# Optimization experiments

Measured on AMD Instinct MI355X. Metric: run time of the kernel, lower is better.

The kernel has to match this reference:

```python
import jax, jax.numpy as jnp
import numpy as np

HEADS = 12
DIM_HEAD = 64
SCALE = DIM_HEAD ** -0.5


def _attn(q, k, v):
    # q: [B, I, D], k/v: [B, J, D]
    sim = jnp.einsum('bid,bjd->bij', q, k)
    a = jax.nn.softmax(sim, axis=-1)
    out = jnp.einsum('bij,bjd->bid', a, v)
    return out, a


def setup_inputs() -> dict:
    key = jax.random.key(0)
    k1, k2, k3 = jax.random.split(key, 3)
    B, F, N, DIM = 8, 8, 196, 768
    x = jax.random.normal(k1, (B, 1 + F * N, DIM), dtype=jnp.float32)
    W_qkv = jax.random.normal(k2, (DIM, 3 * HEADS * DIM_HEAD), dtype=jnp.float32) * (DIM ** -0.5)
    W_out = jax.random.normal(k3, (HEADS * DIM_HEAD, DIM), dtype=jnp.float32) * ((HEADS * DIM_HEAD) ** -0.5)
    b_out = jnp.zeros((DIM,), dtype=jnp.float32)
    return {"x": x, "W_qkv": W_qkv, "W_out": W_out, "b_out": b_out, "f": F}


def reference(x, W_qkv, W_out, b_out, f):
    b, n_tot, dim = x.shape
    h, d = HEADS, DIM_HEAD
    qkv = x @ W_qkv                              # [b, n, 3*h*d]
    q, k, v = jnp.split(qkv, 3, axis=-1)
    # 'b n (h d) -> (b h) n d'
    def to_bh(t):
        return t.reshape(b, n_tot, h, d).transpose(0, 2, 1, 3).reshape(b * h, n_tot, d)
    q, k, v = map(to_bh, (q, k, v))
    q = q * SCALE
    cls_q, q_ = q[:, :1], q[:, 1:]
    cls_k, k_ = k[:, :1], k[:, 1:]
    cls_v, v_ = v[:, :1], v[:, 1:]
    # cls token attends over full sequence
    cls_out, cls_attn = _attn(cls_q, k, v)       # [(b h), 1, d], [(b h), 1, n_tot]
    # spatial attention: 'b (f n) d -> (b f) n d'
    bh = b * h
    n = (n_tot - 1) // f
    def to_bf(t):
        return t.reshape(bh, f, n, d).reshape(bh * f, n, d)
    q_, k_, v_ = map(to_bf, (q_, k_, v_))
    r = f  # q_.shape[0] // cls_k.shape[0]
    # repeat 'b () d -> (b r) () d'
    cls_k_r = jnp.repeat(cls_k, r, axis=0)       # [(bh f), 1, d]
    cls_v_r = jnp.repeat(cls_v, r, axis=0)
    k_ = jnp.concatenate((cls_k_r, k_), axis=1)  # [(bh f), 1+n, d]
    v_ = jnp.concatenate((cls_v_r, v_), axis=1)
    out, _ = _attn(q_, k_, v_)                   # [(bh f), n, d]
    # '(b f) n d -> b (f n) d' (with b := bh)
    out = out.reshape(bh, f * n, d)
    out = jnp.concatenate((cls_out, out), axis=1)  # [(b h), n_tot, d]
    # '(b h) n d -> b n (h d)'
    out = out.reshape(b, h, n_tot, d).transpose(0, 2, 1, 3).reshape(b, n_tot, h * d)
    return out @ W_out + b_out, cls_attn
```

## Files before the change

kernel.cpp:

```cpp
#include <hip/hip_runtime.h>

typedef unsigned short u16;
typedef unsigned int u32;
typedef __attribute__((ext_vector_type(8))) short s16x8;
typedef __attribute__((ext_vector_type(4))) float f32x4;
typedef __attribute__((ext_vector_type(4))) u32 u32x4;
typedef __attribute__((ext_vector_type(4))) float fvec4;

#define DEV static __device__ __forceinline__

typedef __attribute__((address_space(1))) unsigned char ga_u8;
typedef __attribute__((address_space(3))) unsigned char la_u8;

DEV u16 f2bf(float f){
  u32 u = __builtin_bit_cast(u32, f);
  u32 r = (u + 0x7FFFu + ((u >> 16) & 1u)) >> 16;
  return (u16)r;
}
DEV float bf2f(u16 v){
  u32 x = ((u32)v) << 16;
  return __builtin_bit_cast(float, x);
}
DEV f32x4 mfma16(s16x8 a, s16x8 b, f32x4 c){
  return __builtin_amdgcn_mfma_f32_16x16x32_bf16(a, b, c, 0, 0, 0);
}
DEV s16x8 ld16B(const u16* p){
  return __builtin_bit_cast(s16x8, *(const u32x4*)p);
}
DEV u32 cvt_pk_bf16(float lo, float hi){
  u32 r;
  asm("v_cvt_pk_bf16_f32 %0, %1, %2" : "=v"(r) : "v"(lo), "v"(hi));
  return r;
}
DEV void gload16(const void* g, void* l){
  __builtin_amdgcn_global_load_lds((const ga_u8*)g, (la_u8*)l, 16, 0, 0);
}
DEV int xcd_chunk(int bid, int nwg){
  int q = nwg >> 3, r = nwg & 7;
  int xcd = bid & 7, lin = bid >> 3;
  return (xcd < r ? xcd*(q+1) : r*(q+1) + (xcd-r)*q) + lin;
}

#define BARRIER() __builtin_amdgcn_s_barrier()
#define VMC4()    asm volatile("s_waitcnt vmcnt(4)" ::: "memory")
#define VMC0()    asm volatile("s_waitcnt vmcnt(0)" ::: "memory")


__global__ __launch_bounds__(256) void k_prep(const float* __restrict__ x, u16* __restrict__ xb,
                                              const float* __restrict__ Wqkv, u16* __restrict__ wqkvT,
                                              const float* __restrict__ Wout, u16* __restrict__ woutT){
  __shared__ float tile[32][33];
  int b = blockIdx.x, tid = threadIdx.x;
  if (b < 2048){
    const int n4 = 12552*768/4;
    for (int i = b*256 + tid; i < n4; i += 2048*256){
      fvec4 v = ((const fvec4*)x)[i];
      u32 lo = (u32)f2bf(v[0]) | ((u32)f2bf(v[1]) << 16);
      u32 hi = (u32)f2bf(v[2]) | ((u32)f2bf(v[3]) << 16);
      ((u32*)xb)[2*i]   = lo;
      ((u32*)xb)[2*i+1] = hi;
    }
    return;
  }
  const float* W; u16* WT; int K, N, bn, bk;
  if (b < 2048 + 1728){
    int bb = b - 2048; W = Wqkv; WT = wqkvT; K = 768; N = 2304;
    bn = (bb % 72) * 32; bk = (bb / 72) * 32;
  } else {
    int bb = b - 3776; W = Wout; WT = woutT; K = 768; N = 768;
    bn = (bb % 24) * 32; bk = (bb / 24) * 32;
  }
  int tx = tid & 31, ty = tid >> 5;
  #pragma unroll
  for (int r = ty; r < 32; r += 8)
    tile[r][tx] = W[(size_t)(bk + r)*N + bn + tx];
  __syncthreads();
  #pragma unroll
  for (int r = ty; r < 32; r += 8)
    WT[(size_t)(bn + r)*K + bk + tx] = f2bf(tile[tx][r]);
}

__global__ __launch_bounds__(512, 2) void gemm_qkv(const u16* __restrict__ A, const u16* __restrict__ BT,
                                                   u16* __restrict__ qout, u16* __restrict__ kout, u16* __restrict__ vout){
  __shared__ u16 sA[2][2][128*64];
  __shared__ u16 sB[2][2][128*64];
  const int M = 12552;
  const int NWG = 50*9;
  int logical = xcd_chunk(blockIdx.x, NWG);
  int bxi = logical % 9, byi = logical / 9;
  int bm = byi * 256, bn = bxi * 256;

  int tid = threadIdx.x;
  int w = tid >> 6, l = tid & 63, l15 = l & 15, l4 = l >> 4;
  int wm = w >> 2, wn = w & 3;
  int swz = (l15 & 7) << 3;

  f32x4 acc[8][4];
  #pragma unroll
  for (int a=0;a<8;a++)
    #pragma unroll
    for (int b=0;b<4;b++) acc[a][b] = (f32x4){0.f,0.f,0.f,0.f};

  auto stageA = [&](int dbuf, int h, int kt){
    #pragma unroll
    for (int i=0;i<2;i++){
      int ci = i*512 + tid;
      int cs = ci ^ ((ci>>3)&7);
      int r = cs>>3, cc = (cs&7)*8;
      int gr = bm + h*128 + r; if (gr >= M) gr = M-1;
      gload16(A + (size_t)gr*768 + kt*64 + cc, &sA[dbuf][h][(i*512 + (w<<6))*8]);
    }
  };
  auto stageB = [&](int dbuf, int h, int kt){
    #pragma unroll
    for (int i=0;i<2;i++){
      int ci = i*512 + tid;
      int cs = ci ^ ((ci>>3)&7);
      int r = cs>>3, cc = (cs&7)*8;
      gload16(BT + (size_t)(bn + h*128 + r)*768 + kt*64 + cc, &sB[dbuf][h][(i*512 + (w<<6))*8]);
    }
  };

  s16x8 af[4][2], bf[4][2];
  #define LDA_(d, mi, kk) ld16B(&sA[d][wm][(((mi)*16 + l15)*64 + (kk)*32 + l4*8) ^ swz])
  #define LDB_(d, ni, kk) ld16B(&sB[d][(wn*64 + (ni)*16 + l15)>>7][((((wn*64 + (ni)*16 + l15)&127))*64 + (kk)*32 + l4*8) ^ swz])
  #define QUAD(MH, NH) do{ \
    __builtin_amdgcn_s_setprio(1); \
    _Pragma("unroll") \
    for (int j=0;j<4;j++){ \
      _Pragma("unroll") \
      for (int n=0;n<2;n++){ \
        acc[(MH)*4+j][(NH)*2+n] = mfma16(af[j][0], bf[(NH)*2+n][0], acc[(MH)*4+j][(NH)*2+n]); \
        acc[(MH)*4+j][(NH)*2+n] = mfma16(af[j][1], bf[(NH)*2+n][1], acc[(MH)*4+j][(NH)*2+n]); \
      } } \
    __builtin_amdgcn_s_setprio(0); }while(0)

  stageA(0,0,0); stageA(0,1,0); stageB(0,0,0); stageB(0,1,0);
  stageA(1,0,1); stageA(1,1,1);
  VMC4();
  BARRIER();

  #pragma unroll 1
  for (int it = 0; it < 6; ++it){
    int kt1 = 2*it + 1;
    bool full = (it < 5);
    #pragma unroll
    for (int j=0;j<4;j++){ af[j][0]=LDA_(0,j,0); af[j][1]=LDA_(0,j,1); }
    #pragma unroll
    for (int n=0;n<2;n++){ bf[n][0]=LDB_(0,n,0); bf[n][1]=LDB_(0,n,1); }
    stageB(1, 0, kt1);
    BARRIER();
    QUAD(0,0);
    BARRIER();
    #pragma unroll
    for (int n=2;n<4;n++){ bf[n][0]=LDB_(0,n,0); bf[n][1]=LDB_(0,n,1); }
    stageB(1, 1, kt1);
    BARRIER();
    QUAD(0,1);
    BARRIER();
    #pragma unroll
    for (int j=0;j<4;j++){ af[j][0]=LDA_(0,4+j,0); af[j][1]=LDA_(0,4+j,1); }
    if (full){ stageA(0, 0, kt1+1); stageA(0, 1, kt1+1); }
    BARRIER();
    QUAD(1,0); QUAD(1,1);
    if (full) { VMC4(); } else { VMC0(); }
    BARRIER();
    #pragma unroll
    for (int j=0;j<4;j++){ af[j][0]=LDA_(1,j,0); af[j][1]=LDA_(1,j,1); }
    #pragma unroll
    for (int n=0;n<2;n++){ bf[n][0]=LDB_(1,n,0); bf[n][1]=LDB_(1,n,1); }
    if (full) stageB(0, 0, kt1+1);
    BARRIER();
    QUAD(0,0);
    BARRIER();
    #pragma unroll
    for (int n=2;n<4;n++){ bf[n][0]=LDB_(1,n,0); bf[n][1]=LDB_(1,n,1); }
    if (full) stageB(0, 1, kt1+1);
    BARRIER();
    QUAD(0,1);
    BARRIER();
    #pragma unroll
    for (int j=0;j<4;j++){ af[j][0]=LDA_(1,4+j,0); af[j][1]=LDA_(1,4+j,1); }
    if (full){ stageA(1, 0, kt1+2); stageA(1, 1, kt1+2); }
    BARRIER();
    QUAD(1,0); QUAD(1,1);
    if (full) VMC4();
    BARRIER();
  }
  #undef LDA_
  #undef LDB_
  #undef QUAD

  int which = bn / 768;
  int h = ((bn - which*768) >> 6) + wn;
  u16* dst  = (which==0) ? qout : ((which==1) ? kout : vout);
  float scale = (which==0) ? 0.125f : 1.f;
  #pragma unroll
  for (int mi=0; mi<8; mi++){
    #pragma unroll
    for (int r=0; r<4; r++){
      int m = bm + wm*128 + mi*16 + l4*4 + r;
      if (m >= M) continue;
      int b = m / 1569, t = m - b*1569;
      u16* drow = dst + ((size_t)(b*12 + h)*1569 + t)*64 + l15;
      #pragma unroll
      for (int n=0; n<4; n++)
        drow[n*16] = f2bf(acc[mi][n][r] * scale);
    }
  }
}

__global__ __launch_bounds__(256) void cls_a(const u16* __restrict__ qb, const u16* __restrict__ kb,
                                             const u16* __restrict__ vb, float* __restrict__ simw,
                                             float* __restrict__ bsum, float* __restrict__ pvp){
  int bb = blockIdx.x;
  int c = bb % 7, g = bb / 7;
  int tid = threadIdx.x;
  __shared__ float qv[64];
  __shared__ float e_lds[256];
  __shared__ float red[256];
  if (tid < 64) qv[tid] = bf2f(qb[(size_t)g*1569*64 + tid]);
  __syncthreads();
  int j = c*256 + tid;
  float e = 0.f;
  if (j < 1569){
    const u16* kr = kb + ((size_t)g*1569 + j)*64;
    float a = 0.f;
    #pragma unroll
    for (int d0 = 0; d0 < 64; d0 += 8){
      u32x4 u = *(const u32x4*)(kr + d0);
      const u16* us = (const u16*)&u;
      #pragma unroll
      for (int i=0;i<8;i++) a += qv[d0+i]*bf2f(us[i]);
    }
    e = __expf(a - 8.f);
    simw[(size_t)g*1569 + j] = e;
  }
  e_lds[tid] = e;
  red[tid] = e; __syncthreads();
  for (int st=128; st>0; st>>=1){ if (tid<st) red[tid] += red[tid+st]; __syncthreads(); }
  if (tid == 0) bsum[g*8 + c] = red[0];
  int d = tid & 63, kk = tid >> 6;
  float a = 0.f;
  for (int jj = kk; jj < 256; jj += 4){
    int jg = c*256 + jj;
    if (jg < 1569) a += e_lds[jj] * bf2f(vb[((size_t)g*1569+jg)*64 + d]);
  }
  red[tid] = a; __syncthreads();
  if (tid < 64) pvp[((size_t)g*7 + c)*64 + tid] = red[tid]+red[tid+64]+red[tid+128]+red[tid+192];
}

__global__ __launch_bounds__(256, 2) void k_frame(const u16* __restrict__ qb, const u16* __restrict__ kb,
                                                  const u16* __restrict__ vb, u16* __restrict__ ob){
  __shared__ u16 Vt[64][232];
  __shared__ float rs_lds[4][64];

  int g = blockIdx.x, tid = threadIdx.x;
  int bh = g >> 3, fi = g & 7;
  int w = tid >> 6, l = tid & 63;
  int l15 = l & 15, l4 = l >> 4;

  const u16* qg = qb + ((size_t)bh*1569 + 1 + fi*196)*64;
  const u16* kg = kb + (size_t)bh*1569*64;
  const u16* vg = vb + (size_t)bh*1569*64;

  {
    int jj = tid >> 3, c = (tid & 7)*8;
    #pragma unroll
    for (int base = 0; base < 224; base += 32){
      int j = base + jj;
      u32x4 vv = {0,0,0,0};
      if (j < 197){
        int t = (j == 0) ? 0 : (1 + fi*196 + j - 1);
        vv = *(const u32x4*)(vg + (size_t)t*64 + c);
      }
      int jl = j & 31;
      int col = (j & ~31) + ((jl>>2)&3)*8 + (jl>>4)*4 + (jl&3);
      const u16* vp = (const u16*)&vv;
      #pragma unroll
      for (int i=0;i<8;i++) Vt[c+i][col] = vp[i];
    }
  }

  s16x8 qf[4][2];
  #pragma unroll
  for (int mt=0; mt<4; mt++){
    int row = w*64 + mt*16 + l15;
    #pragma unroll
    for (int kk=0; kk<2; kk++){
      if (row < 196) qf[mt][kk] = ld16B(qg + (size_t)row*64 + kk*32 + l4*8);
      else { u32x4 z = {0,0,0,0}; qf[mt][kk] = __builtin_bit_cast(s16x8, z); }
    }
  }

  f32x4 acc[4][4];
  float rsum[4] = {0.f, 0.f, 0.f, 0.f};
  #pragma unroll
  for (int a=0;a<4;a++)
    #pragma unroll
    for (int b=0;b<4;b++) acc[a][b] = (f32x4){0.f,0.f,0.f,0.f};

  __syncthreads();

  #pragma unroll
  for (int ck = 0; ck < 7; ck++){
    int r0 = ck*32 + l15;
    int r1 = r0 + 16;
    int c0 = (r0 < 197 ? r0 : 196);
    int c1 = (r1 < 197 ? r1 : 196);
    int t0 = (r0 == 0) ? 0 : (1 + fi*196 + c0 - 1);
    int t1 = 1 + fi*196 + c1 - 1;
    s16x8 kf0[2], kf1[2];
    #pragma unroll
    for (int kk=0; kk<2; kk++){
      kf0[kk] = ld16B(kg + (size_t)t0*64 + kk*32 + l4*8);
      kf1[kk] = ld16B(kg + (size_t)t1*64 + kk*32 + l4*8);
    }
    s16x8 vf[4];
    #pragma unroll
    for (int ntd=0; ntd<4; ntd++) vf[ntd] = ld16B(&Vt[ntd*16 + l15][ck*32 + l4*8]);
    int kbase = ck*32 + l4*4;

    #define QKPAIR(m, d0, d1) do{ \
      __builtin_amdgcn_s_setprio(1); \
      d0 = (f32x4){0.f,0.f,0.f,0.f}; d1 = (f32x4){0.f,0.f,0.f,0.f}; \
      d0 = mfma16(kf0[0], qf[m][0], d0); \
      d0 = mfma16(kf0[1], qf[m][1], d0); \
      d1 = mfma16(kf1[0], qf[m][0], d1); \
      d1 = mfma16(kf1[1], qf[m][1], d1); \
      __builtin_amdgcn_s_setprio(0); }while(0)

    f32x4 sc0, sc1, nx0, nx1;
    QKPAIR(0, sc0, sc1);
    #pragma unroll
    for (int mt=0; mt<4; mt++){
      if (mt < 3) QKPAIR(mt+1, nx0, nx1);
      float p[8];
      #pragma unroll
      for (int r=0; r<4; r++){
        p[r]   = (kbase + r      < 197) ? __expf(sc0[r] - 8.f) : 0.f;
        p[4+r] = (kbase + 16 + r < 197) ? __expf(sc1[r] - 8.f) : 0.f;
      }
      rsum[mt] += ((p[0]+p[1])+(p[2]+p[3])) + ((p[4]+p[5])+(p[6]+p[7]));
      u32x4 pw;
      pw[0] = cvt_pk_bf16(p[0], p[1]);
      pw[1] = cvt_pk_bf16(p[2], p[3]);
      pw[2] = cvt_pk_bf16(p[4], p[5]);
      pw[3] = cvt_pk_bf16(p[6], p[7]);
      s16x8 pa = __builtin_bit_cast(s16x8, pw);
      __builtin_amdgcn_s_setprio(1);
      #pragma unroll
      for (int ntd=0; ntd<4; ntd++)
        acc[mt][ntd] = mfma16(pa, vf[ntd], acc[mt][ntd]);
      __builtin_amdgcn_s_setprio(0);
      sc0 = nx0; sc1 = nx1;
    }
    #undef QKPAIR
  }

  #pragma unroll
  for (int mt=0; mt<4; mt++){
    float rs = rsum[mt];
    rs += __shfl_xor(rs, 16);
    rs += __shfl_xor(rs, 32);
    rs_lds[w][mt*16 + l15] = rs;
  }

  u16* og = ob + ((size_t)bh*1569 + 1 + fi*196)*64;
  #pragma unroll
  for (int mt=0; mt<4; mt++){
    #pragma unroll
    for (int r=0; r<4; r++){
      int row = w*64 + mt*16 + l4*4 + r;
      if (row < 196){
        float inv = 1.f / rs_lds[w][mt*16 + l4*4 + r];
        #pragma unroll
        for (int ntd=0; ntd<4; ntd++)
          og[(size_t)row*64 + ntd*16 + l15] = f2bf(acc[mt][ntd][r] * inv);
      }
    }
  }
}

__global__ __launch_bounds__(256) void cls_b(const float* __restrict__ simw, const float* __restrict__ bsum,
                                             const float* __restrict__ pvp, float* __restrict__ attn,
                                             u16* __restrict__ ob){
  int bb = blockIdx.x;
  int c = bb % 7, g = bb / 7;
  int tid = threadIdx.x;
  float s = 0.f;
  #pragma unroll
  for (int cc=0;cc<7;cc++) s += bsum[g*8+cc];
  float inv = 1.f/s;
  int j = c*256 + tid;
  if (j < 1569)
    attn[(size_t)g*1569+j] = simw[(size_t)g*1569+j]*inv;
  if (c == 0 && tid < 64){
    float a = 0.f;
    #pragma unroll
    for (int cc=0;cc<7;cc++) a += pvp[((size_t)g*7+cc)*64 + tid];
    ob[(size_t)g*1569*64 + tid] = f2bf(a*inv);
  }
}

__global__ __launch_bounds__(512, 2) void gemm_out(const u16* __restrict__ AO, const u16* __restrict__ BT,
                                                   const float* __restrict__ bias, float* __restrict__ C){
  __shared__ u16 sA[2][2][128*64];
  __shared__ u16 sB[2][2][128*64];
  const int M = 12552;
  const int NWG = 50*3;
  int logical = xcd_chunk(blockIdx.x, NWG);
  int bxi = logical % 3, byi = logical / 3;
  int bm = byi * 256, bn = bxi * 256;

  int tid = threadIdx.x;
  int w = tid >> 6, l = tid & 63, l15 = l & 15, l4 = l >> 4;
  int wm = w >> 2, wn = w & 3;
  int swz = (l15 & 7) << 3;

  f32x4 acc[8][4];
  #pragma unroll
  for (int a=0;a<8;a++)
    #pragma unroll
    for (int b=0;b<4;b++) acc[a][b] = (f32x4){0.f,0.f,0.f,0.f};

  auto stageA = [&](int dbuf, int h, int kt){
    #pragma unroll
    for (int i=0;i<2;i++){
      int ci = i*512 + tid;
      int cs = ci ^ ((ci>>3)&7);
      int r = cs>>3, cc = (cs&7)*8;
      int gr = bm + h*128 + r; if (gr >= M) gr = M-1;
      int b = gr / 1569, t = gr - b*1569;
      gload16(AO + ((size_t)(b*12 + kt)*1569 + t)*64 + cc, &sA[dbuf][h][(i*512 + (w<<6))*8]);
    }
  };
  auto stageB = [&](int dbuf, int h, int kt){
    #pragma unroll
    for (int i=0;i<2;i++){
      int ci = i*512 + tid;
      int cs = ci ^ ((ci>>3)&7);
      int r = cs>>3, cc = (cs&7)*8;
      gload16(BT + (size_t)(bn + h*128 + r)*768 + kt*64 + cc, &sB[dbuf][h][(i*512 + (w<<6))*8]);
    }
  };

  s16x8 af[4][2], bf[4][2];
  #define LDA_(d, mi, kk) ld16B(&sA[d][wm][(((mi)*16 + l15)*64 + (kk)*32 + l4*8) ^ swz])
  #define LDB_(d, ni, kk) ld16B(&sB[d][(wn*64 + (ni)*16 + l15)>>7][((((wn*64 + (ni)*16 + l15)&127))*64 + (kk)*32 + l4*8) ^ swz])
  #define QUAD(MH, NH) do{ \
    __builtin_amdgcn_s_setprio(1); \
    _Pragma("unroll") \
    for (int j=0;j<4;j++){ \
      _Pragma("unroll") \
      for (int n=0;n<2;n++){ \
        acc[(MH)*4+j][(NH)*2+n] = mfma16(af[j][0], bf[(NH)*2+n][0], acc[(MH)*4+j][(NH)*2+n]); \
        acc[(MH)*4+j][(NH)*2+n] = mfma16(af[j][1], bf[(NH)*2+n][1], acc[(MH)*4+j][(NH)*2+n]); \
      } } \
    __builtin_amdgcn_s_setprio(0); }while(0)

  stageA(0,0,0); stageA(0,1,0); stageB(0,0,0); stageB(0,1,0);
  stageA(1,0,1); stageA(1,1,1);
  VMC4();
  BARRIER();

  #pragma unroll 1
  for (int it = 0; it < 6; ++it){
    int kt1 = 2*it + 1;
    bool full = (it < 5);
    #pragma unroll
    for (int j=0;j<4;j++){ af[j][0]=LDA_(0,j,0); af[j][1]=LDA_(0,j,1); }
    #pragma unroll
    for (int n=0;n<2;n++){ bf[n][0]=LDB_(0,n,0); bf[n][1]=LDB_(0,n,1); }
    stageB(1, 0, kt1);
    BARRIER();
    QUAD(0,0);
    BARRIER();
    #pragma unroll
    for (int n=2;n<4;n++){ bf[n][0]=LDB_(0,n,0); bf[n][1]=LDB_(0,n,1); }
    stageB(1, 1, kt1);
    BARRIER();
    QUAD(0,1);
    BARRIER();
    #pragma unroll
    for (int j=0;j<4;j++){ af[j][0]=LDA_(0,4+j,0); af[j][1]=LDA_(0,4+j,1); }
    if (full){ stageA(0, 0, kt1+1); stageA(0, 1, kt1+1); }
    BARRIER();
    QUAD(1,0); QUAD(1,1);
    if (full) { VMC4(); } else { VMC0(); }
    BARRIER();
    #pragma unroll
    for (int j=0;j<4;j++){ af[j][0]=LDA_(1,j,0); af[j][1]=LDA_(1,j,1); }
    #pragma unroll
    for (int n=0;n<2;n++){ bf[n][0]=LDB_(1,n,0); bf[n][1]=LDB_(1,n,1); }
    if (full) stageB(0, 0, kt1+1);
    BARRIER();
    QUAD(0,0);
    BARRIER();
    #pragma unroll
    for (int n=2;n<4;n++){ bf[n][0]=LDB_(1,n,0); bf[n][1]=LDB_(1,n,1); }
    if (full) stageB(0, 1, kt1+1);
    BARRIER();
    QUAD(0,1);
    BARRIER();
    #pragma unroll
    for (int j=0;j<4;j++){ af[j][0]=LDA_(1,4+j,0); af[j][1]=LDA_(1,4+j,1); }
    if (full){ stageA(1, 0, kt1+2); stageA(1, 1, kt1+2); }
    BARRIER();
    QUAD(1,0); QUAD(1,1);
    if (full) VMC4();
    BARRIER();
  }
  #undef LDA_
  #undef LDB_
  #undef QUAD

  int n0 = bn + wn*64;
  float bv[4];
  #pragma unroll
  for (int n=0;n<4;n++) bv[n] = bias[n0 + n*16 + l15];
  #pragma unroll
  for (int mi=0; mi<8; mi++){
    #pragma unroll
    for (int r=0; r<4; r++){
      int m = bm + wm*128 + mi*16 + l4*4 + r;
      if (m >= M) continue;
      float* crow = C + (size_t)m*768 + n0 + l15;
      #pragma unroll
      for (int n=0; n<4; n++)
        crow[n*16] = acc[mi][n][r] + bv[n];
    }
  }
}

extern "C" void kernel_launch(void* const* d_in, const int* in_sizes, int n_in,
                              void* d_out, int out_size, void* d_ws, size_t ws_size,
                              hipStream_t stream){
  (void)in_sizes; (void)n_in; (void)out_size;
  const float* x    = (const float*)d_in[0];
  const float* Wqkv = (const float*)d_in[1];
  const float* Wout = (const float*)d_in[2];
  const float* bout = (const float*)d_in[3];
  float* out0 = (float*)d_out;
  float* out1 = out0 + (size_t)12552*768;

  char* ws = (char*)d_ws;
  size_t off = 0;
  auto alloc = [&](size_t bytes)->char*{
    char* p = ws + off;
    off += (bytes + 255) & ~(size_t)255;
    return p;
  };
  u16* xb    = (u16*)alloc((size_t)12552*768*2);
  u16* wqkvT = (u16*)alloc((size_t)2304*768*2);
  u16* woutT = (u16*)alloc((size_t)768*768*2);
  u16* qb    = (u16*)alloc((size_t)96*1569*64*2);
  u16* kbuf  = (u16*)alloc((size_t)96*1569*64*2);
  u16* vbuf  = (u16*)alloc((size_t)96*1569*64*2);
  u16* ao    = (u16*)alloc((size_t)96*1569*64*2);
  float* simw = (float*)alloc((size_t)96*1569*4);
  float* bsum = (float*)alloc((size_t)96*8*4);
  float* pvp  = (float*)alloc((size_t)96*7*64*4);
  if (off > ws_size) return;

  k_prep<<<4352, 256, 0, stream>>>(x, xb, Wqkv, wqkvT, Wout, woutT);
  gemm_qkv<<<50*9, 512, 0, stream>>>(xb, wqkvT, qb, kbuf, vbuf);
  cls_a<<<672, 256, 0, stream>>>(qb, kbuf, vbuf, simw, bsum, pvp);
  k_frame<<<768, 256, 0, stream>>>(qb, kbuf, vbuf, ao);
  cls_b<<<672, 256, 0, stream>>>(simw, bsum, pvp, out1, ao);
  gemm_out<<<50*3, 512, 0, stream>>>(ao, woutT, bout, out0);
}
```

Before: 162.0 us.

## Merge CLS partial attention into frame attention kernel and hoist B-tile staging

The separate cls_a kernel is folded into the frame attention kernel as extra blocks past index 768, so both independent workloads run in one launch and can fill the GPU together. This removes one launch and the tail gap between the two kernels. Separately, in both GEMMs the second half of the B-tile prefetch is issued together with the first half, earlier in each half-iteration, to give the global loads more time in flight. The merged kernel's shared-memory footprint is now the union of both paths, which may reduce occupancy for the frame blocks.

```diff
diff --git a/kernel.cpp b/kernel.cpp
--- a/kernel.cpp
+++ b/kernel.cpp
@@ -148,13 +148,12 @@
     for (int j=0;j<4;j++){ af[j][0]=LDA_(0,j,0); af[j][1]=LDA_(0,j,1); }
     #pragma unroll
     for (int n=0;n<2;n++){ bf[n][0]=LDB_(0,n,0); bf[n][1]=LDB_(0,n,1); }
-    stageB(1, 0, kt1);
+    stageB(1, 0, kt1); stageB(1, 1, kt1);
     BARRIER();
     QUAD(0,0);
     BARRIER();
     #pragma unroll
     for (int n=2;n<4;n++){ bf[n][0]=LDB_(0,n,0); bf[n][1]=LDB_(0,n,1); }
-    stageB(1, 1, kt1);
     BARRIER();
     QUAD(0,1);
     BARRIER();
@@ -169,13 +168,12 @@
     for (int j=0;j<4;j++){ af[j][0]=LDA_(1,j,0); af[j][1]=LDA_(1,j,1); }
     #pragma unroll
     for (int n=0;n<2;n++){ bf[n][0]=LDB_(1,n,0); bf[n][1]=LDB_(1,n,1); }
-    if (full) stageB(0, 0, kt1+1);
+    if (full){ stageB(0, 0, kt1+1); stageB(0, 1, kt1+1); }
     BARRIER();
     QUAD(0,0);
     BARRIER();
     #pragma unroll
     for (int n=2;n<4;n++){ bf[n][0]=LDB_(1,n,0); bf[n][1]=LDB_(1,n,1); }
-    if (full) stageB(0, 1, kt1+1);
     BARRIER();
     QUAD(0,1);
     BARRIER();
@@ -210,52 +208,54 @@
   }
 }
 
-__global__ __launch_bounds__(256) void cls_a(const u16* __restrict__ qb, const u16* __restrict__ kb,
-                                             const u16* __restrict__ vb, float* __restrict__ simw,
-                                             float* __restrict__ bsum, float* __restrict__ pvp){
-  int bb = blockIdx.x;
-  int c = bb % 7, g = bb / 7;
-  int tid = threadIdx.x;
-  __shared__ float qv[64];
-  __shared__ float e_lds[256];
-  __shared__ float red[256];
-  if (tid < 64) qv[tid] = bf2f(qb[(size_t)g*1569*64 + tid]);
-  __syncthreads();
-  int j = c*256 + tid;
-  float e = 0.f;
-  if (j < 1569){
-    const u16* kr = kb + ((size_t)g*1569 + j)*64;
-    float a = 0.f;
-    #pragma unroll
-    for (int d0 = 0; d0 < 64; d0 += 8){
-      u32x4 u = *(const u32x4*)(kr + d0);
-      const u16* us = (const u16*)&u;
-      #pragma unroll
-      for (int i=0;i<8;i++) a += qv[d0+i]*bf2f(us[i]);
-    }
-    e = __expf(a - 8.f);
-    simw[(size_t)g*1569 + j] = e;
-  }
-  e_lds[tid] = e;
-  red[tid] = e; __syncthreads();
-  for (int st=128; st>0; st>>=1){ if (tid<st) red[tid] += red[tid+st]; __syncthreads(); }
-  if (tid == 0) bsum[g*8 + c] = red[0];
-  int d = tid & 63, kk = tid >> 6;
-  float a = 0.f;
-  for (int jj = kk; jj < 256; jj += 4){
-    int jg = c*256 + jj;
-    if (jg < 1569) a += e_lds[jj] * bf2f(vb[((size_t)g*1569+jg)*64 + d]);
-  }
-  red[tid] = a; __syncthreads();
-  if (tid < 64) pvp[((size_t)g*7 + c)*64 + tid] = red[tid]+red[tid+64]+red[tid+128]+red[tid+192];
-}
-
-__global__ __launch_bounds__(256, 2) void k_frame(const u16* __restrict__ qb, const u16* __restrict__ kb,
-                                                  const u16* __restrict__ vb, u16* __restrict__ ob){
+__global__ __launch_bounds__(256, 2) void k_attn(const u16* __restrict__ qb, const u16* __restrict__ kb,
+                                                 const u16* __restrict__ vb, u16* __restrict__ ob,
+                                                 float* __restrict__ simw, float* __restrict__ bsum,
+                                                 float* __restrict__ pvp){
   __shared__ u16 Vt[64][232];
   __shared__ float rs_lds[4][64];
 
-  int g = blockIdx.x, tid = threadIdx.x;
+  int blk = blockIdx.x, tid = threadIdx.x;
+
+  if (blk >= 768){
+    int bb = blk - 768;
+    int c = bb % 7, g = bb / 7;
+    __shared__ float qv[64];
+    __shared__ float e_lds[256];
+    __shared__ float red[256];
+    if (tid < 64) qv[tid] = bf2f(qb[(size_t)g*1569*64 + tid]);
+    __syncthreads();
+    int j = c*256 + tid;
+    float e = 0.f;
+    if (j < 1569){
+      const u16* kr = kb + ((size_t)g*1569 + j)*64;
+      float a = 0.f;
+      #pragma unroll
+      for (int d0 = 0; d0 < 64; d0 += 8){
+        u32x4 u = *(const u32x4*)(kr + d0);
+        const u16* us = (const u16*)&u;
+        #pragma unroll
+        for (int i=0;i<8;i++) a += qv[d0+i]*bf2f(us[i]);
+      }
+      e = __expf(a - 8.f);
+      simw[(size_t)g*1569 + j] = e;
+    }
+    e_lds[tid] = e;
+    red[tid] = e; __syncthreads();
+    for (int st=128; st>0; st>>=1){ if (tid<st) red[tid] += red[tid+st]; __syncthreads(); }
+    if (tid == 0) bsum[g*8 + c] = red[0];
+    int d = tid & 63, kk = tid >> 6;
+    float a = 0.f;
+    for (int jj = kk; jj < 256; jj += 4){
+      int jg = c*256 + jj;
+      if (jg < 1569) a += e_lds[jj] * bf2f(vb[((size_t)g*1569+jg)*64 + d]);
+    }
+    red[tid] = a; __syncthreads();
+    if (tid < 64) pvp[((size_t)g*7 + c)*64 + tid] = red[tid]+red[tid+64]+red[tid+128]+red[tid+192];
+    return;
+  }
+
+  int g = blk;
   int bh = g >> 3, fi = g & 7;
   int w = tid >> 6, l = tid & 63;
   int l15 = l & 15, l4 = l >> 4;
@@ -472,13 +472,12 @@
     for (int j=0;j<4;j++){ af[j][0]=LDA_(0,j,0); af[j][1]=LDA_(0,j,1); }
     #pragma unroll
     for (int n=0;n<2;n++){ bf[n][0]=LDB_(0,n,0); bf[n][1]=LDB_(0,n,1); }
-    stageB(1, 0, kt1);
+    stageB(1, 0, kt1); stageB(1, 1, kt1);
     BARRIER();
     QUAD(0,0);
     BARRIER();
     #pragma unroll
     for (int n=2;n<4;n++){ bf[n][0]=LDB_(0,n,0); bf[n][1]=LDB_(0,n,1); }
-    stageB(1, 1, kt1);
     BARRIER();
     QUAD(0,1);
     BARRIER();
@@ -493,13 +492,12 @@
     for (int j=0;j<4;j++){ af[j][0]=LDA_(1,j,0); af[j][1]=LDA_(1,j,1); }
     #pragma unroll
     for (int n=0;n<2;n++){ bf[n][0]=LDB_(1,n,0); bf[n][1]=LDB_(1,n,1); }
-    if (full) stageB(0, 0, kt1+1);
+    if (full){ stageB(0, 0, kt1+1); stageB(0, 1, kt1+1); }
     BARRIER();
     QUAD(0,0);
     BARRIER();
     #pragma unroll
     for (int n=2;n<4;n++){ bf[n][0]=LDB_(1,n,0); bf[n][1]=LDB_(1,n,1); }
-    if (full) stageB(0, 1, kt1+1);
     BARRIER();
     QUAD(0,1);
     BARRIER();
@@ -565,8 +563,7 @@
 
   k_prep<<<4352, 256, 0, stream>>>(x, xb, Wqkv, wqkvT, Wout, woutT);
   gemm_qkv<<<50*9, 512, 0, stream>>>(xb, wqkvT, qb, kbuf, vbuf);
-  cls_a<<<672, 256, 0, stream>>>(qb, kbuf, vbuf, simw, bsum, pvp);
-  k_frame<<<768, 256, 0, stream>>>(qb, kbuf, vbuf, ao);
+  k_attn<<<1440, 256, 0, stream>>>(qb, kbuf, vbuf, ao, simw, bsum, pvp);
   cls_b<<<672, 256, 0, stream>>>(simw, bsum, pvp, out1, ao);
   gemm_out<<<50*3, 512, 0, stream>>>(ao, woutT, bout, out0);
 }
```

Measured after the change: 153.3 us, median of 3. 5.4% less time.
